# Performance work log

Measured on AMD Instinct MI355X. Metric: run time of the kernel, lower is better.

Reference implementation:

```python
import jax, jax.numpy as jnp
import numpy as np

TREE = 128
BASIC = 128
EPS = 1e-5


def layer_norm(x, g, b):
    m = jnp.mean(x, axis=-1, keepdims=True)
    v = jnp.mean((x - m) ** 2, axis=-1, keepdims=True)
    return (x - m) * jax.lax.rsqrt(v + EPS) * g + b


def setup_inputs() -> dict:
    key = jax.random.key(0)
    ks = jax.random.split(key, 32)
    n2, n1, n0 = 320000, 80000, 20000
    inp = {
        'subtree_h_top': jax.random.normal(ks[0], (n2, TREE), jnp.float32),
        'atom_x_1': jax.random.normal(ks[1], (n1, BASIC), jnp.float32),
        'atom_x_0': jax.random.normal(ks[2], (n0, BASIC), jnp.float32),
        'bond_x_2': jax.random.normal(ks[3], (n2, BASIC), jnp.float32),
        'bond_x_1': jax.random.normal(ks[4], (n1, BASIC), jnp.float32),
        'branch_W1': jax.random.normal(ks[5], (2, TREE + BASIC, TREE), jnp.float32) * 0.05,
        'branch_b1': jnp.zeros((2, TREE), jnp.float32),
        'branch_g1': jnp.ones((2, TREE), jnp.float32),
        'branch_beta1': jnp.zeros((2, TREE), jnp.float32),
        'branch_W2': jax.random.normal(ks[6], (2, TREE, TREE), jnp.float32) * 0.05,
        'branch_b2': jnp.zeros((2, TREE), jnp.float32),
        'branch_g2': jnp.ones((2, TREE), jnp.float32),
        'branch_beta2': jnp.zeros((2, TREE), jnp.float32),
        'sub_W1': jax.random.normal(ks[7], (2, BASIC + TREE, TREE), jnp.float32) * 0.05,
        'sub_b1': jnp.zeros((2, TREE), jnp.float32),
        'sub_g1': jnp.ones((2, TREE), jnp.float32),
        'sub_beta1': jnp.zeros((2, TREE), jnp.float32),
        'sub_W2': jax.random.normal(ks[8], (2, TREE, TREE), jnp.float32) * 0.05,
        'sub_b2': jnp.zeros((2, TREE), jnp.float32),
        'sub_g2': jnp.ones((2, TREE), jnp.float32),
        'sub_beta2': jnp.zeros((2, TREE), jnp.float32),
        'head_W': jax.random.normal(ks[9], (2, BASIC + TREE, TREE), jnp.float32) * 0.05,
        'head_b': jnp.zeros((2, TREE), jnp.float32),
        'head_g': jnp.ones((2, TREE), jnp.float32),
        'head_beta': jnp.zeros((2, TREE), jnp.float32),
        'src_2': jax.random.randint(ks[10], (n2,), 0, n2),
        'dst_2': jax.random.randint(ks[11], (n2,), 0, n1),
        'src_1': jax.random.randint(ks[12], (n1,), 0, n1),
        'dst_1': jax.random.randint(ks[13], (n1,), 0, n0),
    }
    return inp


def reference(subtree_h_top, atom_x_1, atom_x_0, bond_x_2, bond_x_1,
              branch_W1, branch_b1, branch_g1, branch_beta1,
              branch_W2, branch_b2, branch_g2, branch_beta2,
              sub_W1, sub_b1, sub_g1, sub_beta1,
              sub_W2, sub_b2, sub_g2, sub_beta2,
              head_W, head_b, head_g, head_beta,
              src_2, dst_2, src_1, dst_1):
    relu = jax.nn.relu
    h = subtree_h_top  # subtree_h of level tree_level nodes
    atom_xs = (atom_x_1, atom_x_0)
    bond_xs = (bond_x_2, bond_x_1)
    srcs = (src_2, src_1)
    dsts = (dst_2, dst_1)
    for i in range(2):  # i=0 -> k=2, i=1 -> k=1 (fixed small loop over tree levels)
        ax = atom_xs[i]
        # Branch_Update: edge MLP on [subtree_h[src], bond_x]
        ex = jnp.concatenate([h[srcs[i]], bond_xs[i]], axis=-1)  # [E, tree+basic]
        bh = relu(layer_norm(ex @ branch_W1[i] + branch_b1[i], branch_g1[i], branch_beta1[i]))
        bh = relu(layer_norm(bh @ branch_W2[i] + branch_b2[i], branch_g2[i], branch_beta2[i]))
        # fn.sum aggregation per destination (head) node
        agg = jax.ops.segment_sum(bh, dsts[i], num_segments=ax.shape[0])
        # Tree_Update_Sep
        sx = jnp.concatenate([ax, agg], axis=-1)  # [N, basic+tree]
        f = relu(layer_norm(sx @ sub_W1[i] + sub_b1[i], sub_g1[i], sub_beta1[i]))
        f = relu(layer_norm(f @ sub_W2[i] + sub_b2[i], sub_g2[i], sub_beta2[i]))
        th = jnp.concatenate([ax, f], axis=-1)
        h = relu(layer_norm(th @ head_W[i] + head_b[i], head_g[i], head_beta[i]))
    return h  # subtree_h of atom_0 nodes: [n0, tree_dim]
```

## Files before the change

kernel.cpp:

```cpp
#include <hip/hip_runtime.h>


#define D   128
#define TE  64
#define XS  264

typedef float  f32x4 __attribute__((ext_vector_type(4)));
typedef _Float16 f16x8 __attribute__((ext_vector_type(8)));

__device__ __forceinline__ unsigned short f2h(float f) {
    union { _Float16 h; unsigned short u; } x;
    x.h = (_Float16)f;
    return x.u;
}

__global__ __launch_bounds__(256) void pack_zero(
    const float* __restrict__ brW1, const float* __restrict__ brW2,
    const float* __restrict__ sW1,  const float* __restrict__ sW2,
    const float* __restrict__ hW,   unsigned short* __restrict__ Wp,
    int* __restrict__ cnt, int AN)
{
    int p = blockIdx.x * 256 + threadIdx.x;
    if (p < AN) cnt[p] = 0;
    const float* src; int off, K;
    if (p < 65536)       { src = brW1; off = 0;      K = 256; }
    else if (p < 98304)  { src = brW2; off = 65536;  K = 128; }
    else if (p < 163840) { src = sW1;  off = 98304;  K = 256; }
    else if (p < 196608) { src = sW2;  off = 163840; K = 128; }
    else                 { src = hW;   off = 196608; K = 256; }
    int q = p - off, lvl, r;
    if (K == 256) { lvl = q >> 15; r = q & 32767; }
    else          { lvl = q >> 14; r = q & 16383; }
    int kb = r >> 12, n = (r >> 5) & 127, kk = r & 31;
    Wp[p] = f2h(src[(size_t)lvl * K * 128 + (size_t)(kb * 32 + kk) * 128 + n]);
}


__global__ __launch_bounds__(256) void csr_hist(
    const int* __restrict__ dA, int EA, const int* __restrict__ dB, int EB,
    int* __restrict__ cnt, int AOFFv)
{
    int i = blockIdx.x * 256 + threadIdx.x;
    if (i < EA)               atomicAdd(cnt + dA[i], 1);
    else if (i - EA < EB)     atomicAdd(cnt + AOFFv + dB[i - EA], 1);
}

__global__ __launch_bounds__(256) void csr_scanA(
    const int* __restrict__ cnt, int* __restrict__ inc, int* __restrict__ bsum,
    int nbA, int AOFFv)
{
    __shared__ int lds[256];
    int b = blockIdx.x, t = threadIdx.x;
    int lb, ebase, bs;
    if (b < nbA) { lb = b;       ebase = 0;     bs = lb; }
    else         { lb = b - nbA; ebase = AOFFv; bs = 128 + lb; }
    int idx = ebase + lb * 1024 + t * 4;
    int s0 = cnt[idx], s1 = cnt[idx + 1], s2 = cnt[idx + 2], s3 = cnt[idx + 3];
    int p1 = s0 + s1, p2 = p1 + s2, p3 = p2 + s3;
    lds[t] = p3; __syncthreads();
#pragma unroll
    for (int o = 1; o < 256; o <<= 1) {
        int v = (t >= o) ? lds[t - o] : 0;
        __syncthreads();
        lds[t] += v;
        __syncthreads();
    }
    int ex = lds[t] - p3;
    inc[idx] = ex + s0; inc[idx + 1] = ex + p1; inc[idx + 2] = ex + p2; inc[idx + 3] = ex + p3;
    if (t == 255) bsum[bs] = lds[255];
}

__global__ __launch_bounds__(256) void csr_scanC2(
    const int* __restrict__ cnt, int* __restrict__ inc, const int* __restrict__ bsum,
    int* __restrict__ cursor, int nbA, int nbB, int AOFFv)
{
    __shared__ int lds[256];
    int b = blockIdx.x, t = threadIdx.x;
    int seg = t >> 7, i = t & 127;
    int n = seg ? nbB : nbA;
    lds[t] = (i < n) ? bsum[t] : 0;
    __syncthreads();
#pragma unroll
    for (int o = 1; o < 128; o <<= 1) {
        int v = (i >= o) ? lds[t - o] : 0;
        __syncthreads();
        lds[t] += v;
        __syncthreads();
    }
    int lb, ebase, bs;
    if (b < nbA) { lb = b;       ebase = 0;     bs = lb; }
    else         { lb = b - nbA; ebase = AOFFv; bs = 128 + lb; }
    int carry = (lb > 0) ? lds[bs - 1] : 0;
    int idx = ebase + lb * 1024 + t * 4;
#pragma unroll
    for (int j = 0; j < 4; ++j) {
        int v = inc[idx + j] + carry;
        inc[idx + j] = v;
        cursor[idx + j] = v - cnt[idx + j];
    }
}

__global__ __launch_bounds__(256) void csr_pos(
    const int* __restrict__ dA, int EA, const int* __restrict__ dB, int EB,
    int* __restrict__ cursor, int* __restrict__ posA, int* __restrict__ posB, int AOFFv)
{
    int i = blockIdx.x * 256 + threadIdx.x;
    if (i < EA)           posA[i] = atomicAdd(cursor + dA[i], 1);
    else if (i - EA < EB) posB[i - EA] = atomicAdd(cursor + AOFFv + dB[i - EA], 1);
}


template<int KB>
__device__ __forceinline__ void gemm_f16(const unsigned short* s_in, int stride,
    const unsigned short* __restrict__ Wp, int rb, int cb, int n15, int q, f32x4 acc[2][4])
{
    f32x4 zero = {0.f, 0.f, 0.f, 0.f};
#pragma unroll
    for (int m = 0; m < 2; ++m)
#pragma unroll
        for (int ct = 0; ct < 4; ++ct) acc[m][ct] = zero;
#pragma unroll
    for (int kb = 0; kb < KB; ++kb) {
        f16x8 af0 = *(const f16x8*)(s_in + (rb + n15) * stride + kb * 32 + q * 8);
        f16x8 af1 = *(const f16x8*)(s_in + (rb + 16 + n15) * stride + kb * 32 + q * 8);
        const unsigned short* wb = Wp + (size_t)kb * 4096 + q * 8;
#pragma unroll
        for (int ct = 0; ct < 4; ++ct) {
            f16x8 bf = *(const f16x8*)(wb + (cb + ct * 16 + n15) * 32);
            acc[0][ct] = __builtin_amdgcn_mfma_f32_16x16x32_f16(af0, bf, acc[0][ct], 0, 0, 0);
            acc[1][ct] = __builtin_amdgcn_mfma_f32_16x16x32_f16(af1, bf, acc[1][ct], 0, 0, 0);
        }
    }
}

__device__ __forceinline__ void ln_relu(f32x4 acc[2][4],
    const float* __restrict__ b, const float* __restrict__ g, const float* __restrict__ be,
    float* s_red, float* s_ms, int rb, int cb, int n15, int q, int wcol, int t)
{
#pragma unroll
    for (int ct = 0; ct < 4; ++ct) {
        float bb = b[cb + ct * 16 + n15];
#pragma unroll
        for (int m = 0; m < 2; ++m)
#pragma unroll
            for (int r = 0; r < 4; ++r) acc[m][ct][r] += bb;
    }
    float sum[2][4], ss[2][4];
#pragma unroll
    for (int m = 0; m < 2; ++m)
#pragma unroll
        for (int r = 0; r < 4; ++r) {
            sum[m][r] = acc[m][0][r] + acc[m][1][r] + acc[m][2][r] + acc[m][3][r];
            ss[m][r]  = acc[m][0][r]*acc[m][0][r] + acc[m][1][r]*acc[m][1][r]
                      + acc[m][2][r]*acc[m][2][r] + acc[m][3][r]*acc[m][3][r];
        }
#pragma unroll
    for (int off = 1; off < 16; off <<= 1) {
#pragma unroll
        for (int m = 0; m < 2; ++m)
#pragma unroll
            for (int r = 0; r < 4; ++r) {
                sum[m][r] += __shfl_xor(sum[m][r], off, 64);
                ss[m][r]  += __shfl_xor(ss[m][r],  off, 64);
            }
    }
    if (n15 == 0) {
#pragma unroll
        for (int m = 0; m < 2; ++m)
#pragma unroll
            for (int r = 0; r < 4; ++r) {
                int row = rb + m * 16 + q * 4 + r;
                s_red[row * 4 + wcol * 2 + 0] = sum[m][r];
                s_red[row * 4 + wcol * 2 + 1] = ss[m][r];
            }
    }
    __syncthreads();
    if (t < TE) {
        float sm = s_red[t * 4 + 0] + s_red[t * 4 + 2];
        float sq = s_red[t * 4 + 1] + s_red[t * 4 + 3];
        float mean = sm * (1.f / 128.f);
        float var  = sq * (1.f / 128.f) - mean * mean;
        s_ms[t * 2 + 0] = mean;
        s_ms[t * 2 + 1] = rsqrtf(var + 1e-5f);
    }
    __syncthreads();
#pragma unroll
    for (int ct = 0; ct < 4; ++ct) {
        float gg = g[cb + ct * 16 + n15], bb = be[cb + ct * 16 + n15];
#pragma unroll
        for (int m = 0; m < 2; ++m)
#pragma unroll
            for (int r = 0; r < 4; ++r) {
                int row = rb + m * 16 + q * 4 + r;
                float v = (acc[m][ct][r] - s_ms[row * 2 + 0]) * s_ms[row * 2 + 1] * gg + bb;
                acc[m][ct][r] = fmaxf(v, 0.f);
            }
    }
}

template<bool HBF16, bool CSR>
__global__ __launch_bounds__(256, 4) void edge_mlp(
    const void* __restrict__ hsrc, const float* __restrict__ bond,
    const int* __restrict__ src, const int* __restrict__ dstpos,
    const unsigned short* __restrict__ Wp1, const unsigned short* __restrict__ Wp2,
    const float* __restrict__ b1, const float* __restrict__ g1, const float* __restrict__ be1,
    const float* __restrict__ b2, const float* __restrict__ g2, const float* __restrict__ be2,
    float* __restrict__ agg, unsigned short* __restrict__ ebh, int E)
{
    __shared__ unsigned short s_x[TE * XS];
    __shared__ float s_red[TE * 4];
    __shared__ float s_ms[TE * 2];
    __shared__ int s_src[TE], s_idx[TE];
    unsigned short* s_y = s_x + 128;

    int t = threadIdx.x, eb = blockIdx.x * TE;
    if (t < TE) {
        int ge = eb + t;
        s_src[t] = (ge < E) ? src[ge] : -1;
        s_idx[t] = (ge < E) ? dstpos[ge] : -1;
    }
    __syncthreads();

    if (HBF16) {
        const unsigned short* hp = (const unsigned short*)hsrc;
        for (int c = t; c < TE * 16; c += 256) {
            int row = c >> 4, k8 = c & 15;
            int s = s_src[row];
            uint4 v = make_uint4(0, 0, 0, 0);
            if (s >= 0) v = *(const uint4*)(hp + (size_t)s * 128 + k8 * 8);
            *(uint4*)(s_x + row * XS + k8 * 8) = v;
        }
    } else {
        const float* hp = (const float*)hsrc;
        for (int c = t; c < TE * 32; c += 256) {
            int row = c >> 5, k4 = c & 31;
            int s = s_src[row];
            float4 v = make_float4(0, 0, 0, 0);
            if (s >= 0) v = *(const float4*)(hp + (size_t)s * 128 + k4 * 4);
            ushort4 o; o.x = f2h(v.x); o.y = f2h(v.y); o.z = f2h(v.z); o.w = f2h(v.w);
            *(ushort4*)(s_x + row * XS + k4 * 4) = o;
        }
    }
    for (int c = t; c < TE * 32; c += 256) {
        int row = c >> 5, k4 = c & 31;
        int ge = eb + row;
        float4 v = make_float4(0, 0, 0, 0);
        if (ge < E) v = *(const float4*)(bond + (size_t)ge * 128 + k4 * 4);
        ushort4 o; o.x = f2h(v.x); o.y = f2h(v.y); o.z = f2h(v.z); o.w = f2h(v.w);
        *(ushort4*)(s_x + row * XS + 128 + k4 * 4) = o;
    }
    __syncthreads();

    int l = t & 63, w = t >> 6;
    int n15 = l & 15, q = l >> 4;
    int rb = (w & 1) * 32, cb = (w >> 1) * 64, wcol = w >> 1;

    f32x4 acc[2][4];
    gemm_f16<8>(s_x, XS, Wp1, rb, cb, n15, q, acc);
    ln_relu(acc, b1, g1, be1, s_red, s_ms, rb, cb, n15, q, wcol, t);
#pragma unroll
    for (int m = 0; m < 2; ++m)
#pragma unroll
        for (int ct = 0; ct < 4; ++ct)
#pragma unroll
            for (int r = 0; r < 4; ++r)
                s_y[(rb + m * 16 + q * 4 + r) * XS + cb + ct * 16 + n15] = f2h(acc[m][ct][r]);
    __syncthreads();
    gemm_f16<4>(s_y, XS, Wp2, rb, cb, n15, q, acc);
    ln_relu(acc, b2, g2, be2, s_red, s_ms, rb, cb, n15, q, wcol, t);

    if (CSR) {
#pragma unroll
        for (int m = 0; m < 2; ++m)
#pragma unroll
            for (int ct = 0; ct < 4; ++ct)
#pragma unroll
                for (int r = 0; r < 4; ++r)
                    s_x[(rb + m * 16 + q * 4 + r) * XS + cb + ct * 16 + n15] = f2h(acc[m][ct][r]);
        __syncthreads();
        for (int c = t; c < TE * 16; c += 256) {
            int row = c >> 4, k8 = c & 15;
            int p = s_idx[row];
            if (p >= 0)
                *(uint4*)(ebh + (size_t)p * 128 + k8 * 8) =
                    *(const uint4*)(s_x + row * XS + k8 * 8);
        }
    } else {
#pragma unroll
        for (int m = 0; m < 2; ++m)
#pragma unroll
            for (int ct = 0; ct < 4; ++ct)
#pragma unroll
                for (int r = 0; r < 4; ++r) {
                    int row = rb + m * 16 + q * 4 + r;
                    int gd = s_idx[row];
                    if (gd >= 0)
                        atomicAdd(agg + (size_t)gd * D + cb + ct * 16 + n15, acc[m][ct][r]);
                }
    }
}

template<bool OUT_F16, bool CSR>
__global__ __launch_bounds__(256, 4) void node_mlp(
    const float* __restrict__ ax, const float* __restrict__ agg,
    const int* __restrict__ inc, const unsigned short* __restrict__ ebh,
    const unsigned short* __restrict__ Wp1, const unsigned short* __restrict__ Wp2,
    const unsigned short* __restrict__ Wp3,
    const float* __restrict__ b1, const float* __restrict__ g1, const float* __restrict__ be1,
    const float* __restrict__ b2, const float* __restrict__ g2, const float* __restrict__ be2,
    const float* __restrict__ b3, const float* __restrict__ g3, const float* __restrict__ be3,
    void* __restrict__ out, int N)
{
    __shared__ unsigned short s_x[TE * XS];
    __shared__ float s_red[TE * 4];
    __shared__ float s_ms[TE * 2];
    __shared__ int s_beg[TE], s_end[TE];
    unsigned short* s_y = s_x + 128;

    int t = threadIdx.x, nb = blockIdx.x * TE;

    if (CSR && t < TE) {
        int gr = nb + t, b0 = 0, e0 = 0;
        if (gr < N) { e0 = inc[gr]; b0 = (gr == 0) ? 0 : inc[gr - 1]; }
        s_beg[t] = b0; s_end[t] = e0;
    }

    for (int c = t; c < TE * 32; c += 256) {
        int row = c >> 5, k4 = c & 31;
        int gr = nb + row;
        float4 v = make_float4(0, 0, 0, 0);
        if (gr < N) v = *(const float4*)(ax + (size_t)gr * 128 + k4 * 4);
        ushort4 o; o.x = f2h(v.x); o.y = f2h(v.y); o.z = f2h(v.z); o.w = f2h(v.w);
        *(ushort4*)(s_x + row * XS + k4 * 4) = o;
    }

    if (CSR) {
        __syncthreads();
        int r = t >> 2, s4 = t & 3;
        float a[32];
#pragma unroll
        for (int k = 0; k < 32; ++k) a[k] = 0.f;
        int jb = s_beg[r], je = s_end[r];
        int j = jb;
        for (; j + 2 <= je; j += 2) {
            const unsigned short* rp0 = ebh + (size_t)j * 128 + s4 * 32;
            const unsigned short* rp1 = rp0 + 128;
            f16x8 a0 = *(const f16x8*)rp0;
            f16x8 a1 = *(const f16x8*)(rp0 + 8);
            f16x8 a2 = *(const f16x8*)(rp0 + 16);
            f16x8 a3 = *(const f16x8*)(rp0 + 24);
            f16x8 b0 = *(const f16x8*)rp1;
            f16x8 b1v = *(const f16x8*)(rp1 + 8);
            f16x8 b2v = *(const f16x8*)(rp1 + 16);
            f16x8 b3v = *(const f16x8*)(rp1 + 24);
#pragma unroll
            for (int k = 0; k < 8; ++k) {
                a[k]      += (float)a0[k];
                a[8 + k]  += (float)a1[k];
                a[16 + k] += (float)a2[k];
                a[24 + k] += (float)a3[k];
            }
#pragma unroll
            for (int k = 0; k < 8; ++k) {
                a[k]      += (float)b0[k];
                a[8 + k]  += (float)b1v[k];
                a[16 + k] += (float)b2v[k];
                a[24 + k] += (float)b3v[k];
            }
        }
        if (j < je) {
            const unsigned short* rp = ebh + (size_t)j * 128 + s4 * 32;
            f16x8 v0 = *(const f16x8*)rp;
            f16x8 v1 = *(const f16x8*)(rp + 8);
            f16x8 v2 = *(const f16x8*)(rp + 16);
            f16x8 v3 = *(const f16x8*)(rp + 24);
#pragma unroll
            for (int k = 0; k < 8; ++k) {
                a[k]      += (float)v0[k];
                a[8 + k]  += (float)v1[k];
                a[16 + k] += (float)v2[k];
                a[24 + k] += (float)v3[k];
            }
        }
        unsigned short* op = s_x + r * XS + 128 + s4 * 32;
#pragma unroll
        for (int blk = 0; blk < 4; ++blk) {
            f16x8 h;
#pragma unroll
            for (int k = 0; k < 8; ++k) h[k] = (_Float16)a[blk * 8 + k];
            *(f16x8*)(op + blk * 8) = h;
        }
    } else {
        for (int c = t; c < TE * 32; c += 256) {
            int row = c >> 5, k4 = c & 31;
            int gr = nb + row;
            float4 v = make_float4(0, 0, 0, 0);
            if (gr < N) v = *(const float4*)(agg + (size_t)gr * 128 + k4 * 4);
            ushort4 o; o.x = f2h(v.x); o.y = f2h(v.y); o.z = f2h(v.z); o.w = f2h(v.w);
            *(ushort4*)(s_x + row * XS + 128 + k4 * 4) = o;
        }
    }
    __syncthreads();

    int l = t & 63, w = t >> 6;
    int n15 = l & 15, q = l >> 4;
    int rb = (w & 1) * 32, cb = (w >> 1) * 64, wcol = w >> 1;

    f32x4 acc[2][4];
    gemm_f16<8>(s_x, XS, Wp1, rb, cb, n15, q, acc);
    ln_relu(acc, b1, g1, be1, s_red, s_ms, rb, cb, n15, q, wcol, t);
#pragma unroll
    for (int m = 0; m < 2; ++m)
#pragma unroll
        for (int ct = 0; ct < 4; ++ct)
#pragma unroll
            for (int r = 0; r < 4; ++r)
                s_y[(rb + m * 16 + q * 4 + r) * XS + cb + ct * 16 + n15] = f2h(acc[m][ct][r]);
    __syncthreads();
    gemm_f16<4>(s_y, XS, Wp2, rb, cb, n15, q, acc);
    ln_relu(acc, b2, g2, be2, s_red, s_ms, rb, cb, n15, q, wcol, t);
#pragma unroll
    for (int m = 0; m < 2; ++m)
#pragma unroll
        for (int ct = 0; ct < 4; ++ct)
#pragma unroll
            for (int r = 0; r < 4; ++r)
                s_x[(rb + m * 16 + q * 4 + r) * XS + 128 + cb + ct * 16 + n15] = f2h(acc[m][ct][r]);
    __syncthreads();
    gemm_f16<8>(s_x, XS, Wp3, rb, cb, n15, q, acc);
    ln_relu(acc, b3, g3, be3, s_red, s_ms, rb, cb, n15, q, wcol, t);

#pragma unroll
    for (int m = 0; m < 2; ++m)
#pragma unroll
        for (int ct = 0; ct < 4; ++ct)
#pragma unroll
            for (int r = 0; r < 4; ++r) {
                int row = rb + m * 16 + q * 4 + r;
                int gr = nb + row;
                int col = cb + ct * 16 + n15;
                if (gr < N) {
                    if (OUT_F16)
                        ((unsigned short*)out)[(size_t)gr * D + col] = f2h(acc[m][ct][r]);
                    else
                        ((float*)out)[(size_t)gr * D + col] = acc[m][ct][r];
                }
            }
}

extern "C" void kernel_launch(void* const* d_in, const int* in_sizes, int n_in,
                              void* d_out, int out_size, void* d_ws, size_t ws_size,
                              hipStream_t stream)
{
    const float* h2   = (const float*)d_in[0];
    const float* ax1  = (const float*)d_in[1];
    const float* ax0  = (const float*)d_in[2];
    const float* bx2  = (const float*)d_in[3];
    const float* bx1  = (const float*)d_in[4];
    const float* brW1 = (const float*)d_in[5];
    const float* brb1 = (const float*)d_in[6];
    const float* brg1 = (const float*)d_in[7];
    const float* brbe1= (const float*)d_in[8];
    const float* brW2 = (const float*)d_in[9];
    const float* brb2 = (const float*)d_in[10];
    const float* brg2 = (const float*)d_in[11];
    const float* brbe2= (const float*)d_in[12];
    const float* sW1  = (const float*)d_in[13];
    const float* sb1  = (const float*)d_in[14];
    const float* sg1  = (const float*)d_in[15];
    const float* sbe1 = (const float*)d_in[16];
    const float* sW2  = (const float*)d_in[17];
    const float* sb2  = (const float*)d_in[18];
    const float* sg2  = (const float*)d_in[19];
    const float* sbe2 = (const float*)d_in[20];
    const float* hW   = (const float*)d_in[21];
    const float* hb   = (const float*)d_in[22];
    const float* hg   = (const float*)d_in[23];
    const float* hbe  = (const float*)d_in[24];
    const int*   src2 = (const int*)d_in[25];
    const int*   dst2 = (const int*)d_in[26];
    const int*   src1 = (const int*)d_in[27];
    const int*   dst1 = (const int*)d_in[28];

    int n2 = in_sizes[0] / D;
    int n1 = in_sizes[1] / D;
    int n0 = in_sizes[2] / D;

    unsigned short* Wp = (unsigned short*)d_ws;

    const unsigned short* pBr1[2] = { Wp + 0,      Wp + 32768 };
    const unsigned short* pBr2[2] = { Wp + 65536,  Wp + 65536  + 16384 };
    const unsigned short* pS1 [2] = { Wp + 98304,  Wp + 98304  + 32768 };
    const unsigned short* pS2 [2] = { Wp + 163840, Wp + 163840 + 16384 };
    const unsigned short* pH  [2] = { Wp + 196608, Wp + 196608 + 32768 };

    int nbA = (n1 + 1023) / 1024, nbB = (n0 + 1023) / 1024;
    int AOFFv = nbA * 1024;
    int AN = AOFFv + nbB * 1024;
    auto al = [](size_t x) { return (x + 255) & ~(size_t)255; };
    size_t o = 524288;
    size_t cnt_o  = o; o = al(o + (size_t)AN * 4);
    size_t inc_o  = o; o = al(o + (size_t)AN * 4);
    size_t cur_o  = o; o = al(o + (size_t)AN * 4);
    size_t bsum_o = o; o = al(o + 1024);
    size_t posA_o = o; o = al(o + (size_t)n2 * 4);
    size_t posB_o = o; o = al(o + (size_t)n1 * 4);
    size_t h1_o   = o; o = al(o + (size_t)n1 * 256);
    size_t ebh_o  = o; o = al(o + (size_t)n2 * 256);
    size_t o_csr  = o;
    bool use_csr = (nbA <= 128) && (nbB <= 128) && (ws_size >= o_csr);

    int t2e = (n2 + TE - 1) / TE, t1e = (n1 + TE - 1) / TE;
    int t1n = (n1 + TE - 1) / TE, t0n = (n0 + TE - 1) / TE;

    if (use_csr) {
        int*            cnt    = (int*)((char*)d_ws + cnt_o);
        int*            inc    = (int*)((char*)d_ws + inc_o);
        int*            cursor = (int*)((char*)d_ws + cur_o);
        int*            bsum   = (int*)((char*)d_ws + bsum_o);
        int*            posA   = (int*)((char*)d_ws + posA_o);
        int*            posB   = (int*)((char*)d_ws + posB_o);
        unsigned short* h1     = (unsigned short*)((char*)d_ws + h1_o);
        unsigned short* ebh    = (unsigned short*)((char*)d_ws + ebh_o);

        int EG = (n2 + n1 + 255) / 256;
        pack_zero<<<dim3(1024), dim3(256), 0, stream>>>(brW1, brW2, sW1, sW2, hW, Wp, cnt, AN);
        csr_hist  <<<dim3(EG),        dim3(256), 0, stream>>>(dst2, n2, dst1, n1, cnt, AOFFv);
        csr_scanA <<<dim3(nbA + nbB), dim3(256), 0, stream>>>(cnt, inc, bsum, nbA, AOFFv);
        csr_scanC2<<<dim3(nbA + nbB), dim3(256), 0, stream>>>(cnt, inc, bsum, cursor, nbA, nbB, AOFFv);
        csr_pos   <<<dim3(EG),        dim3(256), 0, stream>>>(dst2, n2, dst1, n1, cursor, posA, posB, AOFFv);

        edge_mlp<false, true><<<dim3(t2e), dim3(256), 0, stream>>>(
            h2, bx2, src2, posA, pBr1[0], pBr2[0],
            brb1, brg1, brbe1, brb2, brg2, brbe2, nullptr, ebh, n2);
        node_mlp<true, true><<<dim3(t1n), dim3(256), 0, stream>>>(
            ax1, nullptr, inc, ebh, pS1[0], pS2[0], pH[0],
            sb1, sg1, sbe1, sb2, sg2, sbe2, hb, hg, hbe, h1, n1);

        edge_mlp<true, true><<<dim3(t1e), dim3(256), 0, stream>>>(
            h1, bx1, src1, posB, pBr1[1], pBr2[1],
            brb1 + D, brg1 + D, brbe1 + D, brb2 + D, brg2 + D, brbe2 + D, nullptr, ebh, n1);
        node_mlp<false, true><<<dim3(t0n), dim3(256), 0, stream>>>(
            ax0, nullptr, inc + AOFFv, ebh, pS1[1], pS2[1], pH[1],
            sb1 + D, sg1 + D, sbe1 + D, sb2 + D, sg2 + D, sbe2 + D,
            hb + D, hg + D, hbe + D, d_out, n0);
    } else {
        float*          agg = (float*)((char*)d_ws + 524288);
        unsigned short* h1  = (unsigned short*)(agg + (size_t)n1 * D);

        pack_zero<<<dim3(1024), dim3(256), 0, stream>>>(brW1, brW2, sW1, sW2, hW, Wp, nullptr, 0);

        hipMemsetAsync(agg, 0, (size_t)n1 * D * sizeof(float), stream);
        edge_mlp<false, false><<<dim3(t2e), dim3(256), 0, stream>>>(
            h2, bx2, src2, dst2, pBr1[0], pBr2[0],
            brb1, brg1, brbe1, brb2, brg2, brbe2, agg, nullptr, n2);
        node_mlp<true, false><<<dim3(t1n), dim3(256), 0, stream>>>(
            ax1, agg, nullptr, nullptr, pS1[0], pS2[0], pH[0],
            sb1, sg1, sbe1, sb2, sg2, sbe2, hb, hg, hbe, h1, n1);

        hipMemsetAsync(agg, 0, (size_t)n0 * D * sizeof(float), stream);
        edge_mlp<true, false><<<dim3(t1e), dim3(256), 0, stream>>>(
            h1, bx1, src1, dst1, pBr1[1], pBr2[1],
            brb1 + D, brg1 + D, brbe1 + D, brb2 + D, brg2 + D, brbe2 + D, agg, nullptr, n1);
        node_mlp<false, false><<<dim3(t0n), dim3(256), 0, stream>>>(
            ax0, agg, nullptr, nullptr, pS1[1], pS2[1], pH[1],
            sb1 + D, sg1 + D, sbe1 + D, sb2 + D, sg2 + D, sbe2 + D,
            hb + D, hg + D, hbe + D, d_out, n0);
    }
}
```

Measured before the change: 675.7 us.

## Add persistent edge MLP kernel with LDS-resident weights and register prefetch

Adds a persistent edge_async kernel that launches 256 blocks. Each block loads both branch weight matrices into swizzled LDS once and then loops over a contiguous chunk of 32-edge tiles. The gathered h rows and bond rows for the next tile are fetched into registers while the current tile runs its two GEMM+LayerNorm stages, then written into a double-buffered LDS tile. This is meant to remove per-tile weight reloads and hide gather latency, at the cost of about 150KB of LDS per block, occupancy of one block per CU, and extra barriers per tile.

```diff
diff --git a/kernel.cpp b/kernel.cpp
--- a/kernel.cpp
+++ b/kernel.cpp
@@ -1,9 +1,11 @@
 #include <hip/hip_runtime.h>
 
 
-#define D   128
-#define TE  64
-#define XS  264
+#define D    128
+#define TE   64
+#define XS   264
+#define TE2  32
+#define MAXT 40
 
 typedef float  f32x4 __attribute__((ext_vector_type(4)));
 typedef _Float16 f16x8 __attribute__((ext_vector_type(8)));
@@ -107,6 +109,280 @@
     int i = blockIdx.x * 256 + threadIdx.x;
     if (i < EA)           posA[i] = atomicAdd(cursor + dA[i], 1);
     else if (i - EA < EB) posB[i - EA] = atomicAdd(cursor + AOFFv + dB[i - EA], 1);
+}
+
+
+__device__ __forceinline__ void ln_relu32(f32x4 acc[4],
+    const float* __restrict__ b, const float* __restrict__ g, const float* __restrict__ be,
+    float* s_red, float* s_ms, int rb, int cb, int n15, int q, int wcol, int t)
+{
+#pragma unroll
+    for (int ct = 0; ct < 4; ++ct) {
+        float bb = b[cb + ct * 16 + n15];
+#pragma unroll
+        for (int r = 0; r < 4; ++r) acc[ct][r] += bb;
+    }
+    float sum[4], ss[4];
+#pragma unroll
+    for (int r = 0; r < 4; ++r) {
+        sum[r] = acc[0][r] + acc[1][r] + acc[2][r] + acc[3][r];
+        ss[r]  = acc[0][r]*acc[0][r] + acc[1][r]*acc[1][r]
+               + acc[2][r]*acc[2][r] + acc[3][r]*acc[3][r];
+    }
+#pragma unroll
+    for (int off = 1; off < 16; off <<= 1) {
+#pragma unroll
+        for (int r = 0; r < 4; ++r) {
+            sum[r] += __shfl_xor(sum[r], off, 64);
+            ss[r]  += __shfl_xor(ss[r],  off, 64);
+        }
+    }
+    if (n15 == 0) {
+#pragma unroll
+        for (int r = 0; r < 4; ++r) {
+            int row = rb + q * 4 + r;
+            s_red[row * 4 + wcol * 2 + 0] = sum[r];
+            s_red[row * 4 + wcol * 2 + 1] = ss[r];
+        }
+    }
+    __syncthreads();
+    if (t < TE2) {
+        float sm = s_red[t * 4 + 0] + s_red[t * 4 + 2];
+        float sq = s_red[t * 4 + 1] + s_red[t * 4 + 3];
+        float mean = sm * (1.f / 128.f);
+        float var  = sq * (1.f / 128.f) - mean * mean;
+        s_ms[t * 2 + 0] = mean;
+        s_ms[t * 2 + 1] = rsqrtf(var + 1e-5f);
+    }
+    __syncthreads();
+#pragma unroll
+    for (int ct = 0; ct < 4; ++ct) {
+        float gg = g[cb + ct * 16 + n15], bb = be[cb + ct * 16 + n15];
+#pragma unroll
+        for (int r = 0; r < 4; ++r) {
+            int row = rb + q * 4 + r;
+            float v = (acc[ct][r] - s_ms[row * 2 + 0]) * s_ms[row * 2 + 1] * gg + bb;
+            acc[ct][r] = fmaxf(v, 0.f);
+        }
+    }
+}
+
+template<bool HBF16>
+__global__ __launch_bounds__(256, 1) void edge_async(
+    const void* __restrict__ hsrc, const float* __restrict__ bond,
+    const int* __restrict__ src, const int* __restrict__ dstpos,
+    const unsigned short* __restrict__ Wp1g, const unsigned short* __restrict__ Wp2g,
+    const float* __restrict__ b1, const float* __restrict__ g1, const float* __restrict__ be1,
+    const float* __restrict__ b2, const float* __restrict__ g2, const float* __restrict__ be2,
+    unsigned short* __restrict__ ebh, int E, int ntiles, int chunk)
+{
+    __shared__ unsigned short s_w1[32768];
+    __shared__ unsigned short s_w2[16384];
+    __shared__ unsigned short s_x[2][8192];
+    __shared__ int   s_meta[MAXT * 64];
+    __shared__ float s_red[TE2 * 4];
+    __shared__ float s_ms[TE2 * 2];
+
+    int t = threadIdx.x;
+    int tile0 = blockIdx.x * chunk;
+    int myT = ntiles - tile0;
+    if (myT > chunk) myT = chunk;
+
+    {
+        const uint4* w1 = (const uint4*)Wp1g;
+        for (int u = t; u < 4096; u += 256) {
+            int kb = u >> 9, l = u & 511, n = l >> 2;
+            *(uint4*)((char*)s_w1 + kb * 8192 + ((l ^ ((n >> 1) & 3)) << 4)) = w1[u];
+        }
+        const uint4* w2 = (const uint4*)Wp2g;
+        for (int u = t; u < 2048; u += 256) {
+            int kb = u >> 9, l = u & 511, n = l >> 2;
+            *(uint4*)((char*)s_w2 + kb * 8192 + ((l ^ ((n >> 1) & 3)) << 4)) = w2[u];
+        }
+        for (int x = t; x < myT * 64; x += 256) {
+            int ti = x >> 6, r = x & 63;
+            int ge = (tile0 + ti) * TE2 + (r & 31);
+            int v;
+            if (r < 32) v = (ge < E) ? src[ge] : 0;
+            else        v = (ge < E) ? dstpos[ge] : -1;
+            s_meta[x] = v;
+        }
+    }
+    __syncthreads();
+    if (myT <= 0) return;
+
+    int r0  = t >> 5, k4 = t & 31;
+    int r0h = t >> 4, k8 = t & 15;
+
+    {
+        if (HBF16) {
+            const unsigned short* hp = (const unsigned short*)hsrc;
+#pragma unroll
+            for (int j = 0; j < 2; ++j) {
+                int row = r0h + 16 * j;
+                int sv = s_meta[row];
+                uint4 v = *(const uint4*)(hp + (size_t)sv * 128 + k8 * 8);
+                *(uint4*)((char*)&s_x[0][0] + row * 512 + ((k8 ^ (row & 7)) << 4)) = v;
+            }
+        } else {
+            const float* hp = (const float*)hsrc;
+#pragma unroll
+            for (int j = 0; j < 4; ++j) {
+                int row = r0 + 8 * j;
+                int sv = s_meta[row];
+                float4 v = *(const float4*)(hp + (size_t)sv * 128 + k4 * 4);
+                ushort4 o; o.x = f2h(v.x); o.y = f2h(v.y); o.z = f2h(v.z); o.w = f2h(v.w);
+                *(ushort4*)((char*)&s_x[0][0] + row * 512
+                            + (((k4 >> 1) ^ (row & 7)) << 4) + (k4 & 1) * 8) = o;
+            }
+        }
+#pragma unroll
+        for (int j = 0; j < 4; ++j) {
+            int row = r0 + 8 * j;
+            int ge = tile0 * TE2 + row;
+            float4 v = make_float4(0, 0, 0, 0);
+            if (ge < E) v = *(const float4*)(bond + (size_t)ge * 128 + k4 * 4);
+            ushort4 o; o.x = f2h(v.x); o.y = f2h(v.y); o.z = f2h(v.z); o.w = f2h(v.w);
+            *(ushort4*)((char*)&s_x[0][0] + row * 512
+                        + (((16 + (k4 >> 1)) ^ (row & 7)) << 4) + (k4 & 1) * 8) = o;
+        }
+    }
+    __syncthreads();
+
+    int lane = t & 63, w = t >> 6;
+    int n15 = lane & 15, q = lane >> 4;
+    int rb = (w & 1) * 16, cb = (w >> 1) * 64, wcol = w >> 1;
+
+    int c = 0;
+    for (int i = 0; i < myT; ++i) {
+        bool hasN = (i + 1 < myT);
+        uint4  nh16[2]; float4 nh32[4]; float4 nb[4];
+        if (hasN) {
+            int mt = i + 1, tb = (tile0 + mt) * TE2;
+            if (HBF16) {
+                const unsigned short* hp = (const unsigned short*)hsrc;
+#pragma unroll
+                for (int j = 0; j < 2; ++j) {
+                    int row = r0h + 16 * j;
+                    int sv = s_meta[mt * 64 + row];
+                    nh16[j] = *(const uint4*)(hp + (size_t)sv * 128 + k8 * 8);
+                }
+            } else {
+                const float* hp = (const float*)hsrc;
+#pragma unroll
+                for (int j = 0; j < 4; ++j) {
+                    int row = r0 + 8 * j;
+                    int sv = s_meta[mt * 64 + row];
+                    nh32[j] = *(const float4*)(hp + (size_t)sv * 128 + k4 * 4);
+                }
+            }
+#pragma unroll
+            for (int j = 0; j < 4; ++j) {
+                int row = r0 + 8 * j, ge = tb + row;
+                nb[j] = make_float4(0, 0, 0, 0);
+                if (ge < E) nb[j] = *(const float4*)(bond + (size_t)ge * 128 + k4 * 4);
+            }
+        }
+
+        const unsigned short* xb = &s_x[c][0];
+        unsigned short* f1b = (unsigned short*)&s_x[c ^ 1][0];
+        unsigned short* f2b = f1b + 4096;
+
+        f32x4 acc[4];
+        f32x4 zero = {0.f, 0.f, 0.f, 0.f};
+#pragma unroll
+        for (int ct = 0; ct < 4; ++ct) acc[ct] = zero;
+#pragma unroll
+        for (int kb = 0; kb < 8; ++kb) {
+            f16x8 af = *(const f16x8*)((const char*)xb + (rb + n15) * 512
+                                       + (((kb * 4 + q) ^ (n15 & 7)) << 4));
+#pragma unroll
+            for (int ct = 0; ct < 4; ++ct) {
+                int n = cb + ct * 16 + n15, l = n * 4 + q;
+                f16x8 bf = *(const f16x8*)((const char*)s_w1 + kb * 8192
+                                           + ((l ^ ((n >> 1) & 3)) << 4));
+                acc[ct] = __builtin_amdgcn_mfma_f32_16x16x32_f16(af, bf, acc[ct], 0, 0, 0);
+            }
+        }
+        ln_relu32(acc, b1, g1, be1, s_red, s_ms, rb, cb, n15, q, wcol, t);
+#pragma unroll
+        for (int ct = 0; ct < 4; ++ct)
+#pragma unroll
+            for (int r = 0; r < 4; ++r) {
+                int row = rb + q * 4 + r, col = cb + ct * 16 + n15;
+                *(unsigned short*)((char*)f1b + row * 256
+                                   + ((col * 2) ^ ((row & 7) << 4))) = f2h(acc[ct][r]);
+            }
+        __syncthreads();
+
+#pragma unroll
+        for (int ct = 0; ct < 4; ++ct) acc[ct] = zero;
+#pragma unroll
+        for (int kb = 0; kb < 4; ++kb) {
+            f16x8 af = *(const f16x8*)((const char*)f1b + (rb + n15) * 256
+                                       + (((kb * 4 + q) ^ (n15 & 7)) << 4));
+#pragma unroll
+            for (int ct = 0; ct < 4; ++ct) {
+                int n = cb + ct * 16 + n15, l = n * 4 + q;
+                f16x8 bf = *(const f16x8*)((const char*)s_w2 + kb * 8192
+                                           + ((l ^ ((n >> 1) & 3)) << 4));
+                acc[ct] = __builtin_amdgcn_mfma_f32_16x16x32_f16(af, bf, acc[ct], 0, 0, 0);
+            }
+        }
+        ln_relu32(acc, b2, g2, be2, s_red, s_ms, rb, cb, n15, q, wcol, t);
+#pragma unroll
+        for (int ct = 0; ct < 4; ++ct)
+#pragma unroll
+            for (int r = 0; r < 4; ++r) {
+                int row = rb + q * 4 + r, col = cb + ct * 16 + n15;
+                *(unsigned short*)((char*)f2b + row * 256
+                                   + ((col * 2) ^ ((row & 7) << 4))) = f2h(acc[ct][r]);
+            }
+        __syncthreads();
+
+#pragma unroll
+        for (int j = 0; j < 2; ++j) {
+            int row = r0h + 16 * j;
+            int p = s_meta[i * 64 + 32 + row];
+            if (p >= 0) {
+                uint4 v = *(const uint4*)((const char*)f2b + row * 256
+                                          + ((k8 ^ (row & 7)) << 4));
+                *(uint4*)(ebh + (size_t)p * 128 + k8 * 8) = v;
+            }
+        }
+        __syncthreads();
+
+        if (hasN) {
+            unsigned short* dstb = (unsigned short*)&s_x[c ^ 1][0];
+            if (HBF16) {
+#pragma unroll
+                for (int j = 0; j < 2; ++j) {
+                    int row = r0h + 16 * j;
+                    *(uint4*)((char*)dstb + row * 512 + ((k8 ^ (row & 7)) << 4)) = nh16[j];
+                }
+            } else {
+#pragma unroll
+                for (int j = 0; j < 4; ++j) {
+                    int row = r0 + 8 * j;
+                    ushort4 o;
+                    o.x = f2h(nh32[j].x); o.y = f2h(nh32[j].y);
+                    o.z = f2h(nh32[j].z); o.w = f2h(nh32[j].w);
+                    *(ushort4*)((char*)dstb + row * 512
+                                + (((k4 >> 1) ^ (row & 7)) << 4) + (k4 & 1) * 8) = o;
+                }
+            }
+#pragma unroll
+            for (int j = 0; j < 4; ++j) {
+                int row = r0 + 8 * j;
+                ushort4 o;
+                o.x = f2h(nb[j].x); o.y = f2h(nb[j].y); o.z = f2h(nb[j].z); o.w = f2h(nb[j].w);
+                *(ushort4*)((char*)dstb + row * 512
+                            + (((16 + (k4 >> 1)) ^ (row & 7)) << 4) + (k4 & 1) * 8) = o;
+            }
+        }
+        __syncthreads();
+        c ^= 1;
+    }
 }
 
 
@@ -530,16 +806,31 @@
         csr_scanC2<<<dim3(nbA + nbB), dim3(256), 0, stream>>>(cnt, inc, bsum, cursor, nbA, nbB, AOFFv);
         csr_pos   <<<dim3(EG),        dim3(256), 0, stream>>>(dst2, n2, dst1, n1, cursor, posA, posB, AOFFv);
 
-        edge_mlp<false, true><<<dim3(t2e), dim3(256), 0, stream>>>(
-            h2, bx2, src2, posA, pBr1[0], pBr2[0],
-            brb1, brg1, brbe1, brb2, brg2, brbe2, nullptr, ebh, n2);
+        int tiles2 = (n2 + TE2 - 1) / TE2, chunk2 = (tiles2 + 255) / 256;
+        int tiles1 = (n1 + TE2 - 1) / TE2, chunk1 = (tiles1 + 255) / 256;
+        bool asy2 = (chunk2 <= MAXT), asy1 = (chunk1 <= MAXT);
+
+        if (asy2)
+            edge_async<false><<<dim3(256), dim3(256), 0, stream>>>(
+                h2, bx2, src2, posA, pBr1[0], pBr2[0],
+                brb1, brg1, brbe1, brb2, brg2, brbe2, ebh, n2, tiles2, chunk2);
+        else
+            edge_mlp<false, true><<<dim3(t2e), dim3(256), 0, stream>>>(
+                h2, bx2, src2, posA, pBr1[0], pBr2[0],
+                brb1, brg1, brbe1, brb2, brg2, brbe2, nullptr, ebh, n2);
         node_mlp<true, true><<<dim3(t1n), dim3(256), 0, stream>>>(
             ax1, nullptr, inc, ebh, pS1[0], pS2[0], pH[0],
             sb1, sg1, sbe1, sb2, sg2, sbe2, hb, hg, hbe, h1, n1);
 
-        edge_mlp<true, true><<<dim3(t1e), dim3(256), 0, stream>>>(
-            h1, bx1, src1, posB, pBr1[1], pBr2[1],
-            brb1 + D, brg1 + D, brbe1 + D, brb2 + D, brg2 + D, brbe2 + D, nullptr, ebh, n1);
+        if (asy1)
+            edge_async<true><<<dim3(256), dim3(256), 0, stream>>>(
+                h1, bx1, src1, posB, pBr1[1], pBr2[1],
+                brb1 + D, brg1 + D, brbe1 + D, brb2 + D, brg2 + D, brbe2 + D,
+                ebh, n1, tiles1, chunk1);
+        else
+            edge_mlp<true, true><<<dim3(t1e), dim3(256), 0, stream>>>(
+                h1, bx1, src1, posB, pBr1[1], pBr2[1],
+                brb1 + D, brg1 + D, brbe1 + D, brb2 + D, brg2 + D, brbe2 + D, nullptr, ebh, n1);
         node_mlp<false, true><<<dim3(t0n), dim3(256), 0, stream>>>(
             ax0, nullptr, inc + AOFFv, ebh, pS1[1], pS2[1], pH[1],
             sb1 + D, sg1 + D, sbe1 + D, sb2 + D, sg2 + D, sbe2 + D,
```

New measurement: 679.4 us. No clear change (+0.5%).
